# Kernel optimization log

Measured on AMD Instinct MI355X. Metric: run time of the kernel, lower is better.

The kernel has to match this reference:

```python
import jax, jax.numpy as jnp
import numpy as np

N, E = 50000, 800000
IN, HID, OUT = 128, 128, 64
H, ED = 4, 3
D = HID // H  # per-head dim = 32


def _w(key, shape):
    fan_in = shape[-1]
    return jax.random.normal(key, shape, dtype=jnp.float32) / np.sqrt(fan_in)


def setup_inputs() -> dict:
    key = jax.random.key(0)
    ks = jax.random.split(key, 32)
    inp = {
        "x": jax.random.normal(ks[0], (N, IN), dtype=jnp.float32),
        "edge_index": jax.random.randint(ks[1], (2, E), 0, N, dtype=jnp.int32),
        "edge_attr": jax.random.normal(ks[2], (E, ED), dtype=jnp.float32),
        # layer 1 TransformerConv (bias=False)
        "Wq1": _w(ks[3], (HID, IN)), "Wk1": _w(ks[4], (HID, IN)),
        "Wv1": _w(ks[5], (HID, IN)), "We1": _w(ks[6], (HID, ED)),
        "Ws1": _w(ks[7], (HID, IN)),
        # layer 1 MLP [HID,HID,HID]
        "M1a": _w(ks[8], (HID, HID)), "b1a": jnp.zeros((HID,), jnp.float32),
        "M1b": _w(ks[9], (HID, HID)), "b1b": jnp.zeros((HID,), jnp.float32),
        # layer 2 TransformerConv
        "Wq2": _w(ks[10], (HID, HID)), "Wk2": _w(ks[11], (HID, HID)),
        "Wv2": _w(ks[12], (HID, HID)), "We2": _w(ks[13], (HID, ED)),
        "Ws2": _w(ks[14], (HID, HID)),
        # layer 2 MLP
        "M2a": _w(ks[15], (HID, HID)), "b2a": jnp.zeros((HID,), jnp.float32),
        "M2b": _w(ks[16], (HID, HID)), "b2b": jnp.zeros((HID,), jnp.float32),
        # final MLP [HID,HID,OUT], plain_last=False
        "Wf1": _w(ks[17], (HID, HID)), "bf1": jnp.zeros((HID,), jnp.float32),
        "Wf2": _w(ks[18], (OUT, HID)), "bf2": jnp.zeros((OUT,), jnp.float32),
    }
    return inp


def _gelu(x):
    return jax.nn.gelu(x, approximate=True)


def _transformer_conv(x, src, dst, edge_attr, Wq, Wk, Wv, We, Ws, n_nodes):
    # PyG TransformerConv: x_j = x[src] (message source), x_i = x[dst] (target)
    q = (x @ Wq.T).reshape(n_nodes, H, D)
    e = (edge_attr @ We.T).reshape(-1, H, D)              # [E,H,D]
    k = (x @ Wk.T).reshape(n_nodes, H, D)[src] + e        # [E,H,D]
    v = (x @ Wv.T).reshape(n_nodes, H, D)[src] + e        # [E,H,D]
    alpha = jnp.einsum("ehd,ehd->eh", q[dst], k) / jnp.float32(np.sqrt(D))
    # segment softmax over incoming edges of each target node
    m = jax.ops.segment_max(alpha, dst, num_segments=n_nodes)  # [N,H]
    m = jnp.where(jnp.isfinite(m), m, 0.0)
    p = jnp.exp(alpha - m[dst])
    s = jax.ops.segment_sum(p, dst, num_segments=n_nodes)      # [N,H]
    a = p / jnp.maximum(s[dst], 1e-16)                         # [E,H]
    out = jax.ops.segment_sum(a[:, :, None] * v, dst, num_segments=n_nodes)
    out = out.reshape(n_nodes, H * D)
    # root_weight=True (default): skip connection through lin_skip (no bias)
    return out + x @ Ws.T


def _mlp2(x, Wa, ba, Wb, bb):
    # PyG MLP with plain_last=False: act after every linear, norm=None
    h = _gelu(x @ Wa.T + ba)
    return _gelu(h @ Wb.T + bb)


def reference(x, edge_index, edge_attr,
              Wq1, Wk1, Wv1, We1, Ws1, M1a, b1a, M1b, b1b,
              Wq2, Wk2, Wv2, We2, Ws2, M2a, b2a, M2b, b2b,
              Wf1, bf1, Wf2, bf2):
    n_nodes = x.shape[0]
    src, dst = edge_index[0], edge_index[1]
    h = _transformer_conv(x, src, dst, edge_attr, Wq1, Wk1, Wv1, We1, Ws1, n_nodes)
    h = h + _mlp2(h, M1a, b1a, M1b, b1b)
    h = _transformer_conv(h, src, dst, edge_attr, Wq2, Wk2, Wv2, We2, Ws2, n_nodes)
    h = h + _mlp2(h, M2a, b2a, M2b, b2b)
    return _mlp2(h, Wf1, bf1, Wf2, bf2)
```

## Files before the change

kernel.cpp:

```cpp
#include <hip/hip_runtime.h>
#include <hip/hip_bf16.h>
#include <math.h>

#define NN 50000
#define NE 800000
#define NPAD 50048
#define BCAP 48

typedef unsigned short u16;
typedef unsigned int u32;
typedef __attribute__((ext_vector_type(8))) short short8;
typedef __attribute__((ext_vector_type(4))) float float4v;

__device__ __forceinline__ float us2f(u16 u) { return __uint_as_float(((unsigned)u) << 16); }
__device__ __forceinline__ float blo(u32 u) { return __uint_as_float(u << 16); }
__device__ __forceinline__ float bhi(u32 u) { return __uint_as_float(u & 0xffff0000u); }
__device__ __forceinline__ u16 f2us(float f) {
    unsigned x = __float_as_uint(f);
    return (u16)((x + 0x7FFFu + ((x >> 16) & 1u)) >> 16);
}
__device__ __forceinline__ float gelu_f(float x) {
    float p = x * x;
    float t = x * fmaf(p, 0.0713548162726f, 1.5957691216057308f);
    float e = __expf(-t);
    return x * __builtin_amdgcn_rcpf(1.0f + e);
}
__device__ __forceinline__ void lds_fence() {
    asm volatile("s_waitcnt lgkmcnt(0)" ::: "memory");
}

__device__ __forceinline__ void loadB(const u16* __restrict__ WP, int tile, int l,
                                      short8& b0, short8& b1, short8& b2, short8& b3) {
    const short8* wp = (const short8*)WP + (size_t)tile * 256 + l;
    b0 = wp[0]; b1 = wp[64]; b2 = wp[128]; b3 = wp[192];
}
__device__ __forceinline__ float4v mfma4(short8 b0, short8 b1, short8 b2, short8 b3,
                                         short8 a0, short8 a1, short8 a2, short8 a3) {
    float4v acc = {0.f, 0.f, 0.f, 0.f};
    acc = __builtin_amdgcn_mfma_f32_16x16x32_bf16(a0, b0, acc, 0, 0, 0);
    acc = __builtin_amdgcn_mfma_f32_16x16x32_bf16(a1, b1, acc, 0, 0, 0);
    acc = __builtin_amdgcn_mfma_f32_16x16x32_bf16(a2, b2, acc, 0, 0, 0);
    acc = __builtin_amdgcn_mfma_f32_16x16x32_bf16(a3, b3, acc, 0, 0, 0);
    return acc;
}
__device__ __forceinline__ short8 addbf(short8 x, short8 y) {
    short8 r;
#pragma unroll
    for (int j = 0; j < 8; ++j) r[j] = (short)f2us(us2f((u16)x[j]) + us2f((u16)y[j]));
    return r;
}


__global__ void k_scatter(const int* __restrict__ srcv, const int* __restrict__ dstv,
                          const float* __restrict__ eattr, int* __restrict__ cursor,
                          int4* __restrict__ rec) {
    int e = blockIdx.x * blockDim.x + threadIdx.x;
    if (e >= NE) return;
    int dst = dstv[e];
    int pos = atomicAdd(&cursor[dst], 1);
    if (pos >= BCAP) return;
    int4 r;
    r.x = srcv[e];
    r.y = __float_as_int(eattr[e * 3 + 0]);
    r.z = __float_as_int(eattr[e * 3 + 1]);
    r.w = __float_as_int(eattr[e * 3 + 2]);
    rec[(size_t)dst * BCAP + pos] = r;
}


struct CvtEnt { const float* s; u16* d; int n; float sc; };
struct CvtTab { CvtEnt e[14]; };
__global__ void k_cvt_w(CvtTab tab) {
    CvtEnt E = tab.e[blockIdx.x >> 3];
    int chunk = blockIdx.x & 7;
    int per = E.n >> 3;
    int lo = chunk * per, hi = lo + per;
    for (int o = lo + threadIdx.x; o < hi; o += blockDim.x) {
        int tile = o >> 11;
        int q = (o >> 9) & 3;
        int l = (o >> 3) & 63;
        int j = o & 7;
        int row = tile * 16 + (l & 15);
        int col = q * 32 + (l >> 4) * 8 + j;
        E.d[o] = f2us(E.s[row * 128 + col] * E.sc);
    }
}


__device__ __forceinline__ void store32(const u16* buf, u16* dst, int r0w, int coff, int l) {
#pragma unroll
    for (int it = 0; it < 8; ++it) {
        int j = it * 64 + l;
        int row = j >> 4, col = (j & 15) * 8;
        *(uint4*)(dst + (size_t)(r0w + row) * 256 + coff + col) = *(const uint4*)&buf[row * 136 + col];
    }
}
__device__ __forceinline__ void read_frags(const u16* buf, int m, int kb,
                                           short8& f0, short8& f1, short8& f2, short8& f3) {
    const u16* p = buf + m * 136 + kb * 8;
    f0 = *(const short8*)(p);
    f1 = *(const short8*)(p + 32);
    f2 = *(const short8*)(p + 64);
    f3 = *(const short8*)(p + 96);
}

__device__ __forceinline__ void qkvs_tail(const u16* __restrict__ Wq,
                                          const short8 (&H)[2][4], u16* my,
                                          u16* __restrict__ QS, u16* __restrict__ KVX,
                                          int r0w, int l, int m, int kb) {
#pragma unroll
    for (int tt = 0; tt < 8; ++tt) {
        short8 b0, b1, b2, b3;
        loadB(Wq, tt, l, b0, b1, b2, b3);
        float4v x0 = mfma4(b0, b1, b2, b3, H[0][0], H[0][1], H[0][2], H[0][3]);
        float4v x1 = mfma4(b0, b1, b2, b3, H[1][0], H[1][1], H[1][2], H[1][3]);
#pragma unroll
        for (int r = 0; r < 4; ++r) {
            my[(kb * 4 + r) * 136 + tt * 16 + m] = f2us(x0[r]);
            my[(16 + kb * 4 + r) * 136 + tt * 16 + m] = f2us(x1[r]);
        }
    }
    lds_fence();
    store32(my, QS, r0w, 0, l);
    lds_fence();
#pragma unroll
    for (int tt = 0; tt < 4; ++tt) {
        short8 b0, b1, b2, b3;
        loadB(Wq, 8 + tt, l, b0, b1, b2, b3);
        float4v x0 = mfma4(b0, b1, b2, b3, H[0][0], H[0][1], H[0][2], H[0][3]);
        float4v x1 = mfma4(b0, b1, b2, b3, H[1][0], H[1][1], H[1][2], H[1][3]);
        int c = tt * 32 + 8 * (m >> 2) + (m & 3);
#pragma unroll
        for (int r = 0; r < 4; ++r) {
            my[(kb * 4 + r) * 136 + c] = f2us(x0[r]);
            my[(16 + kb * 4 + r) * 136 + c] = f2us(x1[r]);
        }
    }
#pragma unroll
    for (int tt = 0; tt < 4; ++tt) {
        short8 b0, b1, b2, b3;
        loadB(Wq, 16 + tt, l, b0, b1, b2, b3);
        float4v x0 = mfma4(b0, b1, b2, b3, H[0][0], H[0][1], H[0][2], H[0][3]);
        float4v x1 = mfma4(b0, b1, b2, b3, H[1][0], H[1][1], H[1][2], H[1][3]);
        int c = tt * 32 + 8 * (m >> 2) + (m & 3) + 4;
#pragma unroll
        for (int r = 0; r < 4; ++r) {
            my[(kb * 4 + r) * 136 + c] = f2us(x0[r]);
            my[(16 + kb * 4 + r) * 136 + c] = f2us(x1[r]);
        }
    }
    lds_fence();
    store32(my, KVX, r0w, 0, l);
    lds_fence();
#pragma unroll
    for (int tt = 0; tt < 4; ++tt) {
        short8 b0, b1, b2, b3;
        loadB(Wq, 12 + tt, l, b0, b1, b2, b3);
        float4v x0 = mfma4(b0, b1, b2, b3, H[0][0], H[0][1], H[0][2], H[0][3]);
        float4v x1 = mfma4(b0, b1, b2, b3, H[1][0], H[1][1], H[1][2], H[1][3]);
        int c = tt * 32 + 8 * (m >> 2) + (m & 3);
#pragma unroll
        for (int r = 0; r < 4; ++r) {
            my[(kb * 4 + r) * 136 + c] = f2us(x0[r]);
            my[(16 + kb * 4 + r) * 136 + c] = f2us(x1[r]);
        }
    }
#pragma unroll
    for (int tt = 0; tt < 4; ++tt) {
        short8 b0, b1, b2, b3;
        loadB(Wq, 20 + tt, l, b0, b1, b2, b3);
        float4v x0 = mfma4(b0, b1, b2, b3, H[0][0], H[0][1], H[0][2], H[0][3]);
        float4v x1 = mfma4(b0, b1, b2, b3, H[1][0], H[1][1], H[1][2], H[1][3]);
        int c = tt * 32 + 8 * (m >> 2) + (m & 3) + 4;
#pragma unroll
        for (int r = 0; r < 4; ++r) {
            my[(kb * 4 + r) * 136 + c] = f2us(x0[r]);
            my[(16 + kb * 4 + r) * 136 + c] = f2us(x1[r]);
        }
    }
    lds_fence();
    store32(my, KVX, r0w, 128, l);
    lds_fence();
#pragma unroll
    for (int tt = 0; tt < 8; ++tt) {
        short8 b0, b1, b2, b3;
        loadB(Wq, 24 + tt, l, b0, b1, b2, b3);
        float4v x0 = mfma4(b0, b1, b2, b3, H[0][0], H[0][1], H[0][2], H[0][3]);
        float4v x1 = mfma4(b0, b1, b2, b3, H[1][0], H[1][1], H[1][2], H[1][3]);
#pragma unroll
        for (int r = 0; r < 4; ++r) {
            my[(kb * 4 + r) * 136 + tt * 16 + m] = f2us(x0[r]);
            my[(16 + kb * 4 + r) * 136 + tt * 16 + m] = f2us(x1[r]);
        }
    }
    lds_fence();
    store32(my, QS, r0w, 128, l);
}


__global__ __launch_bounds__(128, 4) void k_qkvs1(const float* __restrict__ Ain,
                                                  const u16* __restrict__ W,
                                                  u16* __restrict__ QS,
                                                  u16* __restrict__ KVX) {
    __shared__ u16 tile[2][32 * 136];
    int tid = threadIdx.x;
    int l = tid & 63, w = tid >> 6, m = l & 15, kb = l >> 4;
    int r0w = blockIdx.x * 64 + w * 32;
    u16* my = tile[w];

    short8 A[2][4];
#pragma unroll
    for (int s = 0; s < 2; ++s) {
        int row = r0w + s * 16 + m;
        const float* ap = Ain + (size_t)row * 128;
        bool ok = row < NN;
#pragma unroll
        for (int i = 0; i < 4; ++i) {
            short8 r;
            if (ok) {
                const float* p = ap + (kb + i * 4) * 8;
                float4 f0 = *(const float4*)p;
                float4 f1 = *(const float4*)(p + 4);
                r[0]=(short)f2us(f0.x); r[1]=(short)f2us(f0.y); r[2]=(short)f2us(f0.z); r[3]=(short)f2us(f0.w);
                r[4]=(short)f2us(f1.x); r[5]=(short)f2us(f1.y); r[6]=(short)f2us(f1.z); r[7]=(short)f2us(f1.w);
            } else {
#pragma unroll
                for (int j = 0; j < 8; ++j) r[j] = 0;
            }
            A[s][i] = r;
        }
    }

    qkvs_tail(W, A, my, QS, KVX, r0w, l, m, kb);
}


__global__ __launch_bounds__(128, 4) void k_mlp_qkvs(const u16* __restrict__ Ain,
                                                     const u16* __restrict__ Wm,
                                                     const float* __restrict__ bias1,
                                                     const float* __restrict__ bias2,
                                                     const u16* __restrict__ Wq,
                                                     u16* __restrict__ QS,
                                                     u16* __restrict__ KVX) {
    __shared__ u16 t1b[2][32 * 136];
    int tid = threadIdx.x;
    int l = tid & 63, w = tid >> 6, m = l & 15, kb = l >> 4;
    int r0w = blockIdx.x * 64 + w * 32;
    u16* t1 = t1b[w];

    short8 A[2][4];
#pragma unroll
    for (int s = 0; s < 2; ++s) {
        const short8* arow = (const short8*)(Ain + (size_t)(r0w + s * 16 + m) * 128);
#pragma unroll
        for (int i = 0; i < 4; ++i) A[s][i] = arow[kb + i * 4];
    }
#pragma unroll
    for (int tt = 0; tt < 8; ++tt) {
        short8 b0, b1, b2, b3;
        loadB(Wm, tt, l, b0, b1, b2, b3);
        float4v x0 = mfma4(b0, b1, b2, b3, A[0][0], A[0][1], A[0][2], A[0][3]);
        float4v x1 = mfma4(b0, b1, b2, b3, A[1][0], A[1][1], A[1][2], A[1][3]);
        float bv = bias1[tt * 16 + m];
#pragma unroll
        for (int r = 0; r < 4; ++r) {
            t1[(kb * 4 + r) * 136 + tt * 16 + m] = f2us(gelu_f(x0[r] + bv));
            t1[(16 + kb * 4 + r) * 136 + tt * 16 + m] = f2us(gelu_f(x1[r] + bv));
        }
    }
    lds_fence();
    short8 C[2][4];
    read_frags(t1, m, kb, C[0][0], C[0][1], C[0][2], C[0][3]);
    read_frags(t1 + 16 * 136, m, kb, C[1][0], C[1][1], C[1][2], C[1][3]);
    lds_fence();
#pragma unroll
    for (int tt = 0; tt < 8; ++tt) {
        short8 b0, b1, b2, b3;
        loadB(Wm + 16384, tt, l, b0, b1, b2, b3);
        float4v x0 = mfma4(b0, b1, b2, b3, C[0][0], C[0][1], C[0][2], C[0][3]);
        float4v x1 = mfma4(b0, b1, b2, b3, C[1][0], C[1][1], C[1][2], C[1][3]);
        float bv = bias2[tt * 16 + m];
#pragma unroll
        for (int r = 0; r < 4; ++r) {
            t1[(kb * 4 + r) * 136 + tt * 16 + m] = f2us(gelu_f(x0[r] + bv));
            t1[(16 + kb * 4 + r) * 136 + tt * 16 + m] = f2us(gelu_f(x1[r] + bv));
        }
    }
    lds_fence();
    short8 H[2][4];
#pragma unroll
    for (int s = 0; s < 2; ++s) {
        short8 f0, f1, f2, f3;
        read_frags(t1 + s * 16 * 136, m, kb, f0, f1, f2, f3);
        H[s][0] = addbf(f0, A[s][0]);
        H[s][1] = addbf(f1, A[s][1]);
        H[s][2] = addbf(f2, A[s][2]);
        H[s][3] = addbf(f3, A[s][3]);
    }
    lds_fence();

    qkvs_tail(Wq, H, t1, QS, KVX, r0w, l, m, kb);
}


__global__ __launch_bounds__(128, 4) void k_mlp_final(const u16* __restrict__ Ain,
                                                      const u16* __restrict__ Wm,
                                                      const float* __restrict__ bias1,
                                                      const float* __restrict__ bias2,
                                                      const u16* __restrict__ Wf,
                                                      const float* __restrict__ bf1,
                                                      const float* __restrict__ bf2,
                                                      float* __restrict__ outp) {
    __shared__ u16 t1b[2][32 * 136];
    int tid = threadIdx.x;
    int l = tid & 63, w = tid >> 6, m = l & 15, kb = l >> 4;
    int r0w = blockIdx.x * 64 + w * 32;
    u16* t1 = t1b[w];

    short8 A[2][4];
#pragma unroll
    for (int s = 0; s < 2; ++s) {
        const short8* arow = (const short8*)(Ain + (size_t)(r0w + s * 16 + m) * 128);
#pragma unroll
        for (int i = 0; i < 4; ++i) A[s][i] = arow[kb + i * 4];
    }
#pragma unroll
    for (int tt = 0; tt < 8; ++tt) {
        short8 b0, b1, b2, b3;
        loadB(Wm, tt, l, b0, b1, b2, b3);
        float4v x0 = mfma4(b0, b1, b2, b3, A[0][0], A[0][1], A[0][2], A[0][3]);
        float4v x1 = mfma4(b0, b1, b2, b3, A[1][0], A[1][1], A[1][2], A[1][3]);
        float bv = bias1[tt * 16 + m];
#pragma unroll
        for (int r = 0; r < 4; ++r) {
            t1[(kb * 4 + r) * 136 + tt * 16 + m] = f2us(gelu_f(x0[r] + bv));
            t1[(16 + kb * 4 + r) * 136 + tt * 16 + m] = f2us(gelu_f(x1[r] + bv));
        }
    }
    lds_fence();
    short8 C[2][4];
    read_frags(t1, m, kb, C[0][0], C[0][1], C[0][2], C[0][3]);
    read_frags(t1 + 16 * 136, m, kb, C[1][0], C[1][1], C[1][2], C[1][3]);
    lds_fence();
#pragma unroll
    for (int tt = 0; tt < 8; ++tt) {
        short8 b0, b1, b2, b3;
        loadB(Wm + 16384, tt, l, b0, b1, b2, b3);
        float4v x0 = mfma4(b0, b1, b2, b3, C[0][0], C[0][1], C[0][2], C[0][3]);
        float4v x1 = mfma4(b0, b1, b2, b3, C[1][0], C[1][1], C[1][2], C[1][3]);
        float bv = bias2[tt * 16 + m];
#pragma unroll
        for (int r = 0; r < 4; ++r) {
            t1[(kb * 4 + r) * 136 + tt * 16 + m] = f2us(gelu_f(x0[r] + bv));
            t1[(16 + kb * 4 + r) * 136 + tt * 16 + m] = f2us(gelu_f(x1[r] + bv));
        }
    }
    lds_fence();
    short8 H[2][4];
#pragma unroll
    for (int s = 0; s < 2; ++s) {
        short8 f0, f1, f2, f3;
        read_frags(t1 + s * 16 * 136, m, kb, f0, f1, f2, f3);
        H[s][0] = addbf(f0, A[s][0]);
        H[s][1] = addbf(f1, A[s][1]);
        H[s][2] = addbf(f2, A[s][2]);
        H[s][3] = addbf(f3, A[s][3]);
    }
    lds_fence();
#pragma unroll
    for (int tt = 0; tt < 8; ++tt) {
        short8 b0, b1, b2, b3;
        loadB(Wf, tt, l, b0, b1, b2, b3);
        float4v x0 = mfma4(b0, b1, b2, b3, H[0][0], H[0][1], H[0][2], H[0][3]);
        float4v x1 = mfma4(b0, b1, b2, b3, H[1][0], H[1][1], H[1][2], H[1][3]);
        float bv = bf1[tt * 16 + m];
#pragma unroll
        for (int r = 0; r < 4; ++r) {
            t1[(kb * 4 + r) * 136 + tt * 16 + m] = f2us(gelu_f(x0[r] + bv));
            t1[(16 + kb * 4 + r) * 136 + tt * 16 + m] = f2us(gelu_f(x1[r] + bv));
        }
    }
    lds_fence();
    short8 F[2][4];
    read_frags(t1, m, kb, F[0][0], F[0][1], F[0][2], F[0][3]);
    read_frags(t1 + 16 * 136, m, kb, F[1][0], F[1][1], F[1][2], F[1][3]);
    lds_fence();
#pragma unroll
    for (int tt = 0; tt < 4; ++tt) {
        short8 b0, b1, b2, b3;
        loadB(Wf + 16384, tt, l, b0, b1, b2, b3);
        float4v x0 = mfma4(b0, b1, b2, b3, F[0][0], F[0][1], F[0][2], F[0][3]);
        float4v x1 = mfma4(b0, b1, b2, b3, F[1][0], F[1][1], F[1][2], F[1][3]);
        float bv = bf2[tt * 16 + m];
#pragma unroll
        for (int r = 0; r < 4; ++r) {
            t1[(kb * 4 + r) * 136 + tt * 16 + m] = f2us(gelu_f(x0[r] + bv));
            t1[(16 + kb * 4 + r) * 136 + tt * 16 + m] = f2us(gelu_f(x1[r] + bv));
        }
    }
    lds_fence();
#pragma unroll
    for (int it = 0; it < 4; ++it) {
        int j = it * 64 + l;
        int row = j >> 3, col = (j & 7) * 8;
        int grow = r0w + row;
        if (grow < NN) {
            uint4 pk = *(const uint4*)&t1[row * 136 + col];
            const u16* pv = (const u16*)&pk;
            float* po = outp + (size_t)grow * 64 + col;
            float4 o0 = {us2f(pv[0]), us2f(pv[1]), us2f(pv[2]), us2f(pv[3])};
            float4 o1 = {us2f(pv[4]), us2f(pv[5]), us2f(pv[6]), us2f(pv[7])};
            *(float4*)po = o0;
            *(float4*)(po + 4) = o1;
        }
    }
}


__global__ __launch_bounds__(256) void k_conv(const int* __restrict__ cursor,
                                              const int4* __restrict__ rec,
                                              const u16* __restrict__ QS,
                                              const u16* __restrict__ KVX,
                                              const float* __restrict__ We,
                                              u16* __restrict__ out) {
    int n = blockIdx.x * 4 + (threadIdx.x >> 6);
    int l = threadIdx.x & 63;
    int half = l >> 5;
    int li = l & 31;
    int c0 = li * 4;
    const u16* qrow = QS + (size_t)n * 256;
    uint2 qu = *(const uint2*)(qrow + c0);
    uint2 su = *(const uint2*)(qrow + 128 + c0);
    float q0 = blo(qu.x), q1 = bhi(qu.x), q2 = blo(qu.y), q3 = bhi(qu.y);
    float g0, g1, g2;
    {
        const float* wp = We + c0 * 3;
        g0 = fmaf(q3, wp[9],  fmaf(q2, wp[6], fmaf(q1, wp[3], q0 * wp[0])));
        g1 = fmaf(q3, wp[10], fmaf(q2, wp[7], fmaf(q1, wp[4], q0 * wp[1])));
        g2 = fmaf(q3, wp[11], fmaf(q2, wp[8], fmaf(q1, wp[5], q0 * wp[2])));
#pragma unroll
        for (int d = 1; d <= 4; d <<= 1) {
            g0 += __shfl_xor(g0, d);
            g1 += __shfl_xor(g1, d);
            g2 += __shfl_xor(g2, d);
        }
    }
    int cntall = min(cursor[n], BCAP);
    int base = n * BCAP;
    float ss = 0.f, o0 = 0.f, o1 = 0.f, o2 = 0.f, o3 = 0.f, S0 = 0.f, S1 = 0.f, S2 = 0.f;
    const u16* kvb = KVX + li * 8;

    auto edge = [&](int4 r, uint4 kv) {
        float part = fmaf(q3, bhi(kv.y), fmaf(q2, blo(kv.y), fmaf(q1, bhi(kv.x), q0 * blo(kv.x))));
        part += __shfl_xor(part, 1);
        part += __shfl_xor(part, 2);
        part += __shfl_xor(part, 4);
        float ea0 = __int_as_float(r.y), ea1 = __int_as_float(r.z), ea2 = __int_as_float(r.w);
        float alpha = fmaf(ea2, g2, fmaf(ea1, g1, fmaf(ea0, g0, part)));
        float p = __expf(fminf(alpha, 80.f));
        o0 = fmaf(p, blo(kv.z), o0);
        o1 = fmaf(p, bhi(kv.z), o1);
        o2 = fmaf(p, blo(kv.w), o2);
        o3 = fmaf(p, bhi(kv.w), o3);
        ss += p;
        S0 = fmaf(p, ea0, S0);
        S1 = fmaf(p, ea1, S1);
        S2 = fmaf(p, ea2, S2);
    };

    int e = base + half;
    int cnt = (half < cntall) ? ((cntall - half + 1) >> 1) : 0;
    if (cnt & 1) {
        int4 r = rec[e];
        uint4 kv = *(const uint4*)(kvb + (u32)(r.x * 256));
        edge(r, kv);
        e += 2;
    }
    for (int i = 0; i < (cnt >> 1); ++i, e += 4) {
        int4 ra = rec[e], rb = rec[e + 2];
        uint4 kva = *(const uint4*)(kvb + (u32)(ra.x * 256));
        uint4 kvb2 = *(const uint4*)(kvb + (u32)(rb.x * 256));
        edge(ra, kva);
        edge(rb, kvb2);
    }
    o0 += __shfl_xor(o0, 32);
    o1 += __shfl_xor(o1, 32);
    o2 += __shfl_xor(o2, 32);
    o3 += __shfl_xor(o3, 32);
    ss += __shfl_xor(ss, 32);
    S0 += __shfl_xor(S0, 32);
    S1 += __shfl_xor(S1, 32);
    S2 += __shfl_xor(S2, 32);
    if (half == 0) {
        float inv = __builtin_amdgcn_rcpf(fmaxf(ss, 1e-16f));
        const float* wp = We + c0 * 3;
        o0 = fmaf(wp[2],  S2, fmaf(wp[1],  S1, fmaf(wp[0], S0, o0)));
        o1 = fmaf(wp[5],  S2, fmaf(wp[4],  S1, fmaf(wp[3], S0, o1)));
        o2 = fmaf(wp[8],  S2, fmaf(wp[7],  S1, fmaf(wp[6], S0, o2)));
        o3 = fmaf(wp[11], S2, fmaf(wp[10], S1, fmaf(wp[9], S0, o3)));
        float r0v = fmaf(o0, inv, blo(su.x));
        float r1v = fmaf(o1, inv, bhi(su.x));
        float r2v = fmaf(o2, inv, blo(su.y));
        float r3v = fmaf(o3, inv, bhi(su.y));
        uint2 ou;
        ou.x = (u32)f2us(r0v) | ((u32)f2us(r1v) << 16);
        ou.y = (u32)f2us(r2v) | ((u32)f2us(r3v) << 16);
        *(uint2*)(out + (size_t)n * 128 + c0) = ou;
    }
}


extern "C" void kernel_launch(void* const* d_in, const int* in_sizes, int n_in,
                              void* d_out, int out_size, void* d_ws, size_t ws_size,
                              hipStream_t stream) {
    const float* x = (const float*)d_in[0];
    const int* ei = (const int*)d_in[1];
    const float* eattr = (const float*)d_in[2];
    const float* Wq1 = (const float*)d_in[3];
    const float* Wk1 = (const float*)d_in[4];
    const float* Wv1 = (const float*)d_in[5];
    const float* We1 = (const float*)d_in[6];
    const float* Ws1 = (const float*)d_in[7];
    const float* M1a = (const float*)d_in[8];
    const float* b1a = (const float*)d_in[9];
    const float* M1b = (const float*)d_in[10];
    const float* b1b = (const float*)d_in[11];
    const float* Wq2 = (const float*)d_in[12];
    const float* Wk2 = (const float*)d_in[13];
    const float* Wv2 = (const float*)d_in[14];
    const float* We2 = (const float*)d_in[15];
    const float* Ws2 = (const float*)d_in[16];
    const float* M2a = (const float*)d_in[17];
    const float* b2a = (const float*)d_in[18];
    const float* M2b = (const float*)d_in[19];
    const float* b2b = (const float*)d_in[20];
    const float* Wf1 = (const float*)d_in[21];
    const float* bf1 = (const float*)d_in[22];
    const float* Wf2 = (const float*)d_in[23];
    const float* bf2 = (const float*)d_in[24];

    char* ws = (char*)d_ws;
    size_t off = 0;
    auto alloc = [&](size_t bytes) -> void* {
        void* p = ws + off;
        off = (off + bytes + 255) & ~(size_t)255;
        return p;
    };
    int* cursor = (int*)alloc((size_t)NN * 4);
    int4* rec = (int4*)alloc((size_t)NN * BCAP * 16);
    u16* QS = (u16*)alloc((size_t)NPAD * 256 * 2);
    u16* KVX = (u16*)alloc((size_t)NPAD * 256 * 2);
    u16* Ha = (u16*)alloc((size_t)NPAD * 128 * 2);
    u16* WB[14];
    const int wsz[14] = {16384, 16384, 16384, 16384, 16384, 16384, 16384,
                         16384, 16384, 16384, 16384, 16384, 16384, 8192};
    for (int i = 0; i < 14; ++i) WB[i] = (u16*)alloc((size_t)wsz[i] * 2);

    const int* srcv = ei;
    const int* dstv = ei + NE;

    hipMemsetAsync(cursor, 0, (size_t)NN * 4, stream);
    k_scatter<<<(NE + 255) / 256, 256, 0, stream>>>(srcv, dstv, eattr, cursor, rec);

    CvtTab tab;
    const float* wsrc[14] = {Wq1, Wk1, Wv1, Ws1, Wq2, Wk2, Wv2, Ws2,
                             M1a, M1b, M2a, M2b, Wf1, Wf2};
    const float SC = 0.17677669529663687f;
    for (int i = 0; i < 14; ++i) {
        tab.e[i].s = wsrc[i];
        tab.e[i].d = WB[i];
        tab.e[i].n = wsz[i];
        tab.e[i].sc = (i == 0 || i == 4) ? SC : 1.0f;
    }
    k_cvt_w<<<112, 256, 0, stream>>>(tab);

    dim3 blk(128);
    dim3 grd(NPAD / 64);
    dim3 gconv(NN / 4);

    k_qkvs1<<<grd, blk, 0, stream>>>(x, WB[0], QS, KVX);
    k_conv<<<gconv, dim3(256), 0, stream>>>(cursor, rec, QS, KVX, We1, Ha);
    k_mlp_qkvs<<<grd, blk, 0, stream>>>(Ha, WB[8], b1a, b1b, WB[4], QS, KVX);
    k_conv<<<gconv, dim3(256), 0, stream>>>(cursor, rec, QS, KVX, We2, Ha);
    k_mlp_final<<<grd, blk, 0, stream>>>(Ha, WB[10], b2a, b2b, WB[12], bf1, bf2, (float*)d_out);
}
```

Baseline: 371.4 us.

## Fuse edge scatter into projection kernel and interleave Q/KV/S into one buffer

The cursor memset moves into the weight-conversion kernel, and the edge-bucketing scatter is merged into the first projection kernel as extra blocks, which cuts the launch count. The Q, KV and skip projections now go into one interleaved 512-wide row per node, so the conv kernel reads q, s and the gathered kv from the same buffer. The node tile per block shrinks from 64 to 32 rows, with the two waves splitting output columns and synchronising with __syncthreads instead of working as independent waves. This doubles the block count and adds barriers, and the scatter blocks now run alongside the GEMM blocks and compete with them for resources.

```diff
diff --git a/kernel.cpp b/kernel.cpp
--- a/kernel.cpp
+++ b/kernel.cpp
@@ -6,6 +6,8 @@
 #define NE 800000
 #define NPAD 50048
 #define BCAP 48
+#define NQB 1564
+#define NSB 6250
 
 typedef unsigned short u16;
 typedef unsigned int u32;
@@ -24,9 +26,6 @@
     float t = x * fmaf(p, 0.0713548162726f, 1.5957691216057308f);
     float e = __expf(-t);
     return x * __builtin_amdgcn_rcpf(1.0f + e);
-}
-__device__ __forceinline__ void lds_fence() {
-    asm volatile("s_waitcnt lgkmcnt(0)" ::: "memory");
 }
 
 __device__ __forceinline__ void loadB(const u16* __restrict__ WP, int tile, int l,
@@ -51,26 +50,10 @@
 }
 
 
-__global__ void k_scatter(const int* __restrict__ srcv, const int* __restrict__ dstv,
-                          const float* __restrict__ eattr, int* __restrict__ cursor,
-                          int4* __restrict__ rec) {
-    int e = blockIdx.x * blockDim.x + threadIdx.x;
-    if (e >= NE) return;
-    int dst = dstv[e];
-    int pos = atomicAdd(&cursor[dst], 1);
-    if (pos >= BCAP) return;
-    int4 r;
-    r.x = srcv[e];
-    r.y = __float_as_int(eattr[e * 3 + 0]);
-    r.z = __float_as_int(eattr[e * 3 + 1]);
-    r.w = __float_as_int(eattr[e * 3 + 2]);
-    rec[(size_t)dst * BCAP + pos] = r;
-}
-
-
 struct CvtEnt { const float* s; u16* d; int n; float sc; };
 struct CvtTab { CvtEnt e[14]; };
-__global__ void k_cvt_w(CvtTab tab) {
+__global__ void k_cvt_w(CvtTab tab, int* __restrict__ cursor) {
+    for (int i = blockIdx.x * 256 + threadIdx.x; i < NN; i += 112 * 256) cursor[i] = 0;
     CvtEnt E = tab.e[blockIdx.x >> 3];
     int chunk = blockIdx.x & 7;
     int per = E.n >> 3;
@@ -87,12 +70,12 @@
 }
 
 
-__device__ __forceinline__ void store32(const u16* buf, u16* dst, int r0w, int coff, int l) {
-#pragma unroll
-    for (int it = 0; it < 8; ++it) {
-        int j = it * 64 + l;
+__device__ __forceinline__ void storeB32(const u16* buf, u16* dst, int r0, int coff, int tid) {
+#pragma unroll
+    for (int it = 0; it < 4; ++it) {
+        int j = it * 128 + tid;
         int row = j >> 4, col = (j & 15) * 8;
-        *(uint4*)(dst + (size_t)(r0w + row) * 256 + coff + col) = *(const uint4*)&buf[row * 136 + col];
+        *(uint4*)(dst + (size_t)(r0 + row) * 512 + coff + col) = *(const uint4*)&buf[row * 136 + col];
     }
 }
 __device__ __forceinline__ void read_frags(const u16* buf, int m, int kb,
@@ -103,115 +86,117 @@
     f2 = *(const short8*)(p + 64);
     f3 = *(const short8*)(p + 96);
 }
+__device__ __forceinline__ void stage2(u16* my, int kb, int cidx, float4v x0, float4v x1) {
+#pragma unroll
+    for (int r = 0; r < 4; ++r) {
+        my[(kb * 4 + r) * 136 + cidx] = f2us(x0[r]);
+        my[(16 + kb * 4 + r) * 136 + cidx] = f2us(x1[r]);
+    }
+}
 
 __device__ __forceinline__ void qkvs_tail(const u16* __restrict__ Wq,
                                           const short8 (&H)[2][4], u16* my,
-                                          u16* __restrict__ QS, u16* __restrict__ KVX,
-                                          int r0w, int l, int m, int kb) {
-#pragma unroll
-    for (int tt = 0; tt < 8; ++tt) {
+                                          u16* __restrict__ QKVS,
+                                          int r0, int tid, int wv, int l, int m, int kb) {
+#pragma unroll
+    for (int i = 0; i < 4; ++i) {
+        int tt = wv * 4 + i;
         short8 b0, b1, b2, b3;
         loadB(Wq, tt, l, b0, b1, b2, b3);
         float4v x0 = mfma4(b0, b1, b2, b3, H[0][0], H[0][1], H[0][2], H[0][3]);
         float4v x1 = mfma4(b0, b1, b2, b3, H[1][0], H[1][1], H[1][2], H[1][3]);
-#pragma unroll
-        for (int r = 0; r < 4; ++r) {
-            my[(kb * 4 + r) * 136 + tt * 16 + m] = f2us(x0[r]);
-            my[(16 + kb * 4 + r) * 136 + tt * 16 + m] = f2us(x1[r]);
-        }
-    }
-    lds_fence();
-    store32(my, QS, r0w, 0, l);
-    lds_fence();
-#pragma unroll
-    for (int tt = 0; tt < 4; ++tt) {
-        short8 b0, b1, b2, b3;
-        loadB(Wq, 8 + tt, l, b0, b1, b2, b3);
-        float4v x0 = mfma4(b0, b1, b2, b3, H[0][0], H[0][1], H[0][2], H[0][3]);
-        float4v x1 = mfma4(b0, b1, b2, b3, H[1][0], H[1][1], H[1][2], H[1][3]);
-        int c = tt * 32 + 8 * (m >> 2) + (m & 3);
-#pragma unroll
-        for (int r = 0; r < 4; ++r) {
-            my[(kb * 4 + r) * 136 + c] = f2us(x0[r]);
-            my[(16 + kb * 4 + r) * 136 + c] = f2us(x1[r]);
-        }
-    }
-#pragma unroll
-    for (int tt = 0; tt < 4; ++tt) {
-        short8 b0, b1, b2, b3;
-        loadB(Wq, 16 + tt, l, b0, b1, b2, b3);
-        float4v x0 = mfma4(b0, b1, b2, b3, H[0][0], H[0][1], H[0][2], H[0][3]);
-        float4v x1 = mfma4(b0, b1, b2, b3, H[1][0], H[1][1], H[1][2], H[1][3]);
-        int c = tt * 32 + 8 * (m >> 2) + (m & 3) + 4;
-#pragma unroll
-        for (int r = 0; r < 4; ++r) {
-            my[(kb * 4 + r) * 136 + c] = f2us(x0[r]);
-            my[(16 + kb * 4 + r) * 136 + c] = f2us(x1[r]);
-        }
-    }
-    lds_fence();
-    store32(my, KVX, r0w, 0, l);
-    lds_fence();
-#pragma unroll
-    for (int tt = 0; tt < 4; ++tt) {
-        short8 b0, b1, b2, b3;
-        loadB(Wq, 12 + tt, l, b0, b1, b2, b3);
-        float4v x0 = mfma4(b0, b1, b2, b3, H[0][0], H[0][1], H[0][2], H[0][3]);
-        float4v x1 = mfma4(b0, b1, b2, b3, H[1][0], H[1][1], H[1][2], H[1][3]);
-        int c = tt * 32 + 8 * (m >> 2) + (m & 3);
-#pragma unroll
-        for (int r = 0; r < 4; ++r) {
-            my[(kb * 4 + r) * 136 + c] = f2us(x0[r]);
-            my[(16 + kb * 4 + r) * 136 + c] = f2us(x1[r]);
-        }
-    }
-#pragma unroll
-    for (int tt = 0; tt < 4; ++tt) {
-        short8 b0, b1, b2, b3;
-        loadB(Wq, 20 + tt, l, b0, b1, b2, b3);
-        float4v x0 = mfma4(b0, b1, b2, b3, H[0][0], H[0][1], H[0][2], H[0][3]);
-        float4v x1 = mfma4(b0, b1, b2, b3, H[1][0], H[1][1], H[1][2], H[1][3]);
-        int c = tt * 32 + 8 * (m >> 2) + (m & 3) + 4;
-#pragma unroll
-        for (int r = 0; r < 4; ++r) {
-            my[(kb * 4 + r) * 136 + c] = f2us(x0[r]);
-            my[(16 + kb * 4 + r) * 136 + c] = f2us(x1[r]);
-        }
-    }
-    lds_fence();
-    store32(my, KVX, r0w, 128, l);
-    lds_fence();
-#pragma unroll
-    for (int tt = 0; tt < 8; ++tt) {
+        stage2(my, kb, tt * 16 + m, x0, x1);
+    }
+    __syncthreads();
+    storeB32(my, QKVS, r0, 0, tid);
+    __syncthreads();
+#pragma unroll
+    for (int i = 0; i < 2; ++i) {
+        int tk = wv * 2 + i;
+        short8 b0, b1, b2, b3;
+        loadB(Wq, 8 + tk, l, b0, b1, b2, b3);
+        float4v x0 = mfma4(b0, b1, b2, b3, H[0][0], H[0][1], H[0][2], H[0][3]);
+        float4v x1 = mfma4(b0, b1, b2, b3, H[1][0], H[1][1], H[1][2], H[1][3]);
+        stage2(my, kb, tk * 32 + 8 * (m >> 2) + (m & 3), x0, x1);
+    }
+#pragma unroll
+    for (int i = 0; i < 2; ++i) {
+        int tk = wv * 2 + i;
+        short8 b0, b1, b2, b3;
+        loadB(Wq, 16 + tk, l, b0, b1, b2, b3);
+        float4v x0 = mfma4(b0, b1, b2, b3, H[0][0], H[0][1], H[0][2], H[0][3]);
+        float4v x1 = mfma4(b0, b1, b2, b3, H[1][0], H[1][1], H[1][2], H[1][3]);
+        stage2(my, kb, tk * 32 + 8 * (m >> 2) + (m & 3) + 4, x0, x1);
+    }
+    __syncthreads();
+    storeB32(my, QKVS, r0, 128, tid);
+    __syncthreads();
+#pragma unroll
+    for (int i = 0; i < 2; ++i) {
+        int tk = wv * 2 + i;
+        short8 b0, b1, b2, b3;
+        loadB(Wq, 12 + tk, l, b0, b1, b2, b3);
+        float4v x0 = mfma4(b0, b1, b2, b3, H[0][0], H[0][1], H[0][2], H[0][3]);
+        float4v x1 = mfma4(b0, b1, b2, b3, H[1][0], H[1][1], H[1][2], H[1][3]);
+        stage2(my, kb, tk * 32 + 8 * (m >> 2) + (m & 3), x0, x1);
+    }
+#pragma unroll
+    for (int i = 0; i < 2; ++i) {
+        int tk = wv * 2 + i;
+        short8 b0, b1, b2, b3;
+        loadB(Wq, 20 + tk, l, b0, b1, b2, b3);
+        float4v x0 = mfma4(b0, b1, b2, b3, H[0][0], H[0][1], H[0][2], H[0][3]);
+        float4v x1 = mfma4(b0, b1, b2, b3, H[1][0], H[1][1], H[1][2], H[1][3]);
+        stage2(my, kb, tk * 32 + 8 * (m >> 2) + (m & 3) + 4, x0, x1);
+    }
+    __syncthreads();
+    storeB32(my, QKVS, r0, 256, tid);
+    __syncthreads();
+#pragma unroll
+    for (int i = 0; i < 4; ++i) {
+        int tt = wv * 4 + i;
         short8 b0, b1, b2, b3;
         loadB(Wq, 24 + tt, l, b0, b1, b2, b3);
         float4v x0 = mfma4(b0, b1, b2, b3, H[0][0], H[0][1], H[0][2], H[0][3]);
         float4v x1 = mfma4(b0, b1, b2, b3, H[1][0], H[1][1], H[1][2], H[1][3]);
-#pragma unroll
-        for (int r = 0; r < 4; ++r) {
-            my[(kb * 4 + r) * 136 + tt * 16 + m] = f2us(x0[r]);
-            my[(16 + kb * 4 + r) * 136 + tt * 16 + m] = f2us(x1[r]);
-        }
-    }
-    lds_fence();
-    store32(my, QS, r0w, 128, l);
-}
-
-
-__global__ __launch_bounds__(128, 4) void k_qkvs1(const float* __restrict__ Ain,
+        stage2(my, kb, tt * 16 + m, x0, x1);
+    }
+    __syncthreads();
+    storeB32(my, QKVS, r0, 384, tid);
+}
+
+
+__global__ __launch_bounds__(128, 4) void k_build(const float* __restrict__ Ain,
                                                   const u16* __restrict__ W,
-                                                  u16* __restrict__ QS,
-                                                  u16* __restrict__ KVX) {
-    __shared__ u16 tile[2][32 * 136];
+                                                  u16* __restrict__ QKVS,
+                                                  const int* __restrict__ srcv,
+                                                  const int* __restrict__ dstv,
+                                                  const float* __restrict__ eattr,
+                                                  int* __restrict__ cursor,
+                                                  int4* __restrict__ rec) {
+    __shared__ u16 tile[32 * 136];
+    if (blockIdx.x >= NQB) {
+        int e = (blockIdx.x - NQB) * 128 + threadIdx.x;
+        if (e >= NE) return;
+        int dst = dstv[e];
+        int pos = atomicAdd(&cursor[dst], 1);
+        if (pos >= BCAP) return;
+        int4 r;
+        r.x = srcv[e];
+        r.y = __float_as_int(eattr[e * 3 + 0]);
+        r.z = __float_as_int(eattr[e * 3 + 1]);
+        r.w = __float_as_int(eattr[e * 3 + 2]);
+        rec[(size_t)dst * BCAP + pos] = r;
+        return;
+    }
     int tid = threadIdx.x;
-    int l = tid & 63, w = tid >> 6, m = l & 15, kb = l >> 4;
-    int r0w = blockIdx.x * 64 + w * 32;
-    u16* my = tile[w];
+    int l = tid & 63, wv = tid >> 6, m = l & 15, kb = l >> 4;
+    int r0 = blockIdx.x * 32;
 
     short8 A[2][4];
 #pragma unroll
     for (int s = 0; s < 2; ++s) {
-        int row = r0w + s * 16 + m;
+        int row = r0 + s * 16 + m;
         const float* ap = Ain + (size_t)row * 128;
         bool ok = row < NN;
 #pragma unroll
@@ -231,7 +216,7 @@
         }
     }
 
-    qkvs_tail(W, A, my, QS, KVX, r0w, l, m, kb);
+    qkvs_tail(W, A, tile, QKVS, r0, tid, wv, l, m, kb);
 }
 
 
@@ -240,23 +225,22 @@
                                                      const float* __restrict__ bias1,
                                                      const float* __restrict__ bias2,
                                                      const u16* __restrict__ Wq,
-                                                     u16* __restrict__ QS,
-                                                     u16* __restrict__ KVX) {
-    __shared__ u16 t1b[2][32 * 136];
+                                                     u16* __restrict__ QKVS) {
+    __shared__ u16 t1[32 * 136];
     int tid = threadIdx.x;
-    int l = tid & 63, w = tid >> 6, m = l & 15, kb = l >> 4;
-    int r0w = blockIdx.x * 64 + w * 32;
-    u16* t1 = t1b[w];
+    int l = tid & 63, wv = tid >> 6, m = l & 15, kb = l >> 4;
+    int r0 = blockIdx.x * 32;
 
     short8 A[2][4];
 #pragma unroll
     for (int s = 0; s < 2; ++s) {
-        const short8* arow = (const short8*)(Ain + (size_t)(r0w + s * 16 + m) * 128);
+        const short8* arow = (const short8*)(Ain + (size_t)(r0 + s * 16 + m) * 128);
 #pragma unroll
         for (int i = 0; i < 4; ++i) A[s][i] = arow[kb + i * 4];
     }
 #pragma unroll
-    for (int tt = 0; tt < 8; ++tt) {
+    for (int i = 0; i < 4; ++i) {
+        int tt = wv * 4 + i;
         short8 b0, b1, b2, b3;
         loadB(Wm, tt, l, b0, b1, b2, b3);
         float4v x0 = mfma4(b0, b1, b2, b3, A[0][0], A[0][1], A[0][2], A[0][3]);
@@ -268,13 +252,14 @@
             t1[(16 + kb * 4 + r) * 136 + tt * 16 + m] = f2us(gelu_f(x1[r] + bv));
         }
     }
-    lds_fence();
+    __syncthreads();
     short8 C[2][4];
     read_frags(t1, m, kb, C[0][0], C[0][1], C[0][2], C[0][3]);
     read_frags(t1 + 16 * 136, m, kb, C[1][0], C[1][1], C[1][2], C[1][3]);
-    lds_fence();
-#pragma unroll
-    for (int tt = 0; tt < 8; ++tt) {
+    __syncthreads();
+#pragma unroll
+    for (int i = 0; i < 4; ++i) {
+        int tt = wv * 4 + i;
         short8 b0, b1, b2, b3;
         loadB(Wm + 16384, tt, l, b0, b1, b2, b3);
         float4v x0 = mfma4(b0, b1, b2, b3, C[0][0], C[0][1], C[0][2], C[0][3]);
@@ -286,7 +271,7 @@
             t1[(16 + kb * 4 + r) * 136 + tt * 16 + m] = f2us(gelu_f(x1[r] + bv));
         }
     }
-    lds_fence();
+    __syncthreads();
     short8 H[2][4];
 #pragma unroll
     for (int s = 0; s < 2; ++s) {
@@ -297,9 +282,9 @@
         H[s][2] = addbf(f2, A[s][2]);
         H[s][3] = addbf(f3, A[s][3]);
     }
-    lds_fence();
-
-    qkvs_tail(Wq, H, t1, QS, KVX, r0w, l, m, kb);
+    __syncthreads();
+
+    qkvs_tail(Wq, H, t1, QKVS, r0, tid, wv, l, m, kb);
 }
 
 
@@ -311,21 +296,21 @@
                                                       const float* __restrict__ bf1,
                                                       const float* __restrict__ bf2,
                                                       float* __restrict__ outp) {
-    __shared__ u16 t1b[2][32 * 136];
+    __shared__ u16 t1[32 * 136];
     int tid = threadIdx.x;
-    int l = tid & 63, w = tid >> 6, m = l & 15, kb = l >> 4;
-    int r0w = blockIdx.x * 64 + w * 32;
-    u16* t1 = t1b[w];
+    int l = tid & 63, wv = tid >> 6, m = l & 15, kb = l >> 4;
+    int r0 = blockIdx.x * 32;
 
     short8 A[2][4];
 #pragma unroll
     for (int s = 0; s < 2; ++s) {
-        const short8* arow = (const short8*)(Ain + (size_t)(r0w + s * 16 + m) * 128);
+        const short8* arow = (const short8*)(Ain + (size_t)(r0 + s * 16 + m) * 128);
 #pragma unroll
         for (int i = 0; i < 4; ++i) A[s][i] = arow[kb + i * 4];
     }
 #pragma unroll
-    for (int tt = 0; tt < 8; ++tt) {
+    for (int i = 0; i < 4; ++i) {
+        int tt = wv * 4 + i;
         short8 b0, b1, b2, b3;
         loadB(Wm, tt, l, b0, b1, b2, b3);
         float4v x0 = mfma4(b0, b1, b2, b3, A[0][0], A[0][1], A[0][2], A[0][3]);
@@ -337,13 +322,14 @@
             t1[(16 + kb * 4 + r) * 136 + tt * 16 + m] = f2us(gelu_f(x1[r] + bv));
         }
     }
-    lds_fence();
+    __syncthreads();
     short8 C[2][4];
     read_frags(t1, m, kb, C[0][0], C[0][1], C[0][2], C[0][3]);
     read_frags(t1 + 16 * 136, m, kb, C[1][0], C[1][1], C[1][2], C[1][3]);
-    lds_fence();
-#pragma unroll
-    for (int tt = 0; tt < 8; ++tt) {
+    __syncthreads();
+#pragma unroll
+    for (int i = 0; i < 4; ++i) {
+        int tt = wv * 4 + i;
         short8 b0, b1, b2, b3;
         loadB(Wm + 16384, tt, l, b0, b1, b2, b3);
         float4v x0 = mfma4(b0, b1, b2, b3, C[0][0], C[0][1], C[0][2], C[0][3]);
@@ -355,7 +341,7 @@
             t1[(16 + kb * 4 + r) * 136 + tt * 16 + m] = f2us(gelu_f(x1[r] + bv));
         }
     }
-    lds_fence();
+    __syncthreads();
     short8 H[2][4];
 #pragma unroll
     for (int s = 0; s < 2; ++s) {
@@ -366,9 +352,10 @@
         H[s][2] = addbf(f2, A[s][2]);
         H[s][3] = addbf(f3, A[s][3]);
     }
-    lds_fence();
-#pragma unroll
-    for (int tt = 0; tt < 8; ++tt) {
+    __syncthreads();
+#pragma unroll
+    for (int i = 0; i < 4; ++i) {
+        int tt = wv * 4 + i;
         short8 b0, b1, b2, b3;
         loadB(Wf, tt, l, b0, b1, b2, b3);
         float4v x0 = mfma4(b0, b1, b2, b3, H[0][0], H[0][1], H[0][2], H[0][3]);
@@ -380,13 +367,14 @@
             t1[(16 + kb * 4 + r) * 136 + tt * 16 + m] = f2us(gelu_f(x1[r] + bv));
         }
     }
-    lds_fence();
+    __syncthreads();
     short8 F[2][4];
     read_frags(t1, m, kb, F[0][0], F[0][1], F[0][2], F[0][3]);
     read_frags(t1 + 16 * 136, m, kb, F[1][0], F[1][1], F[1][2], F[1][3]);
-    lds_fence();
-#pragma unroll
-    for (int tt = 0; tt < 4; ++tt) {
+    __syncthreads();
+#pragma unroll
+    for (int i = 0; i < 2; ++i) {
+        int tt = wv * 2 + i;
         short8 b0, b1, b2, b3;
         loadB(Wf + 16384, tt, l, b0, b1, b2, b3);
         float4v x0 = mfma4(b0, b1, b2, b3, F[0][0], F[0][1], F[0][2], F[0][3]);
@@ -398,12 +386,12 @@
             t1[(16 + kb * 4 + r) * 136 + tt * 16 + m] = f2us(gelu_f(x1[r] + bv));
         }
     }
-    lds_fence();
-#pragma unroll
-    for (int it = 0; it < 4; ++it) {
-        int j = it * 64 + l;
+    __syncthreads();
+#pragma unroll
+    for (int it = 0; it < 2; ++it) {
+        int j = it * 128 + tid;
         int row = j >> 3, col = (j & 7) * 8;
-        int grow = r0w + row;
+        int grow = r0 + row;
         if (grow < NN) {
             uint4 pk = *(const uint4*)&t1[row * 136 + col];
             const u16* pv = (const u16*)&pk;
@@ -419,18 +407,17 @@
 
 __global__ __launch_bounds__(256) void k_conv(const int* __restrict__ cursor,
                                               const int4* __restrict__ rec,
-                                              const u16* __restrict__ QS,
-                                              const u16* __restrict__ KVX,
+                                              const u16* __restrict__ qkvs,
                                               const float* __restrict__ We,
                                               u16* __restrict__ out) {
     int n = blockIdx.x * 4 + (threadIdx.x >> 6);
     int l = threadIdx.x & 63;
     int half = l >> 5;
     int li = l & 31;
-    int c0 = li * 4;
-    const u16* qrow = QS + (size_t)n * 256;
+    int c0 = (li >> 3) * 32 + (li & 7) * 4;
+    const u16* qrow = qkvs + (size_t)n * 512;
     uint2 qu = *(const uint2*)(qrow + c0);
-    uint2 su = *(const uint2*)(qrow + 128 + c0);
+    uint2 su = *(const uint2*)(qrow + 384 + c0);
     float q0 = blo(qu.x), q1 = bhi(qu.x), q2 = blo(qu.y), q3 = bhi(qu.y);
     float g0, g1, g2;
     {
@@ -448,7 +435,7 @@
     int cntall = min(cursor[n], BCAP);
     int base = n * BCAP;
     float ss = 0.f, o0 = 0.f, o1 = 0.f, o2 = 0.f, o3 = 0.f, S0 = 0.f, S1 = 0.f, S2 = 0.f;
-    const u16* kvb = KVX + li * 8;
+    int kvoff = 128 + li * 8;
 
     auto edge = [&](int4 r, uint4 kv) {
         float part = fmaf(q3, bhi(kv.y), fmaf(q2, blo(kv.y), fmaf(q1, bhi(kv.x), q0 * blo(kv.x))));
@@ -472,16 +459,16 @@
     int cnt = (half < cntall) ? ((cntall - half + 1) >> 1) : 0;
     if (cnt & 1) {
         int4 r = rec[e];
-        uint4 kv = *(const uint4*)(kvb + (u32)(r.x * 256));
+        uint4 kv = *(const uint4*)(qkvs + (size_t)r.x * 512 + kvoff);
         edge(r, kv);
         e += 2;
     }
     for (int i = 0; i < (cnt >> 1); ++i, e += 4) {
         int4 ra = rec[e], rb = rec[e + 2];
-        uint4 kva = *(const uint4*)(kvb + (u32)(ra.x * 256));
-        uint4 kvb2 = *(const uint4*)(kvb + (u32)(rb.x * 256));
+        uint4 kva = *(const uint4*)(qkvs + (size_t)ra.x * 512 + kvoff);
+        uint4 kvb = *(const uint4*)(qkvs + (size_t)rb.x * 512 + kvoff);
         edge(ra, kva);
-        edge(rb, kvb2);
+        edge(rb, kvb);
     }
     o0 += __shfl_xor(o0, 32);
     o1 += __shfl_xor(o1, 32);
@@ -548,8 +535,7 @@
     };
     int* cursor = (int*)alloc((size_t)NN * 4);
     int4* rec = (int4*)alloc((size_t)NN * BCAP * 16);
-    u16* QS = (u16*)alloc((size_t)NPAD * 256 * 2);
-    u16* KVX = (u16*)alloc((size_t)NPAD * 256 * 2);
+    u16* QKVS = (u16*)alloc((size_t)NPAD * 512 * 2);
     u16* Ha = (u16*)alloc((size_t)NPAD * 128 * 2);
     u16* WB[14];
     const int wsz[14] = {16384, 16384, 16384, 16384, 16384, 16384, 16384,
@@ -558,9 +544,6 @@
 
     const int* srcv = ei;
     const int* dstv = ei + NE;
-
-    hipMemsetAsync(cursor, 0, (size_t)NN * 4, stream);
-    k_scatter<<<(NE + 255) / 256, 256, 0, stream>>>(srcv, dstv, eattr, cursor, rec);
 
     CvtTab tab;
     const float* wsrc[14] = {Wq1, Wk1, Wv1, Ws1, Wq2, Wk2, Wv2, Ws2,
@@ -572,15 +555,15 @@
         tab.e[i].n = wsz[i];
         tab.e[i].sc = (i == 0 || i == 4) ? SC : 1.0f;
     }
-    k_cvt_w<<<112, 256, 0, stream>>>(tab);
+    k_cvt_w<<<112, 256, 0, stream>>>(tab, cursor);
 
     dim3 blk(128);
-    dim3 grd(NPAD / 64);
+    dim3 grd(NQB);
     dim3 gconv(NN / 4);
 
-    k_qkvs1<<<grd, blk, 0, stream>>>(x, WB[0], QS, KVX);
-    k_conv<<<gconv, dim3(256), 0, stream>>>(cursor, rec, QS, KVX, We1, Ha);
-    k_mlp_qkvs<<<grd, blk, 0, stream>>>(Ha, WB[8], b1a, b1b, WB[4], QS, KVX);
-    k_conv<<<gconv, dim3(256), 0, stream>>>(cursor, rec, QS, KVX, We2, Ha);
+    k_build<<<NQB + NSB, blk, 0, stream>>>(x, WB[0], QKVS, srcv, dstv, eattr, cursor, rec);
+    k_conv<<<gconv, dim3(256), 0, stream>>>(cursor, rec, QKVS, We1, Ha);
+    k_mlp_qkvs<<<grd, blk, 0, stream>>>(Ha, WB[8], b1a, b1b, WB[4], QKVS);
+    k_conv<<<gconv, dim3(256), 0, stream>>>(cursor, rec, QKVS, We2, Ha);
     k_mlp_final<<<grd, blk, 0, stream>>>(Ha, WB[10], b2a, b2b, WB[12], bf1, bf2, (float*)d_out);
 }
```

Measured after the change: 344.6 us. 1.08x faster.
